# Performance work log

Hardware: AMD Instinct MI355X
Metric: run time of the kernel (lower is better)

The kernel has to match this reference:

```python
import jax, jax.numpy as jnp
import numpy as np

NUM_HEADS = 16
KV_CHANNELS = 128
MASK_FILL = -10000.0  # TE attention_mask_func fill value


def setup_inputs() -> dict:
    key = jax.random.key(0)
    k1, k2, k3 = jax.random.split(key, 3)
    S, B, H = 2048, 2, 2048
    hidden_states = jax.random.normal(k1, (S, B, H), dtype=jnp.float32)
    attention_mask = jnp.zeros((B, 1, S, S), dtype=bool)  # True = masked out
    qkv_weight = jax.random.normal(k2, (H, 3 * H), dtype=jnp.float32) * (1.0 / np.sqrt(H))
    qkv_bias = jnp.zeros((3 * H,), dtype=jnp.float32)
    proj_weight = jax.random.normal(k3, (H, H), dtype=jnp.float32) * (1.0 / np.sqrt(H))
    proj_bias = jnp.zeros((H,), dtype=jnp.float32)
    return {
        "hidden_states": hidden_states,
        "attention_mask": attention_mask,
        "qkv_weight": qkv_weight,
        "qkv_bias": qkv_bias,
        "proj_weight": proj_weight,
        "proj_bias": proj_bias,
    }


def reference(hidden_states, attention_mask, qkv_weight, qkv_bias, proj_weight, proj_bias):
    S, B, H = hidden_states.shape
    nh, d = NUM_HEADS, KV_CHANNELS
    # QKV GEMM: [s,b,H] @ [H,3H] -> [s,b,3H] -> [s,b,nh,3d] -> split
    mixed = hidden_states @ qkv_weight + qkv_bias
    mixed = mixed.reshape(S, B, nh, 3 * d)
    q, k, v = jnp.split(mixed, 3, axis=-1)  # each [s,b,nh,d]
    # BMM1 with 1/sqrt(d) scaling (layer_number=None -> no layer scaling)
    norm_factor = jnp.asarray(np.sqrt(d), dtype=hidden_states.dtype)
    scores = jnp.einsum("sbhd,tbhd->bhst", q, k) / norm_factor  # [b,nh,s,s]
    # causal mask (future positions masked) OR'd with provided bool padding mask
    causal = ~jnp.tril(jnp.ones((S, S), dtype=bool))  # True above diagonal
    mask = jnp.logical_or(causal[None, None], attention_mask)
    scores = jnp.where(mask, jnp.asarray(MASK_FILL, scores.dtype), scores)
    probs = jax.nn.softmax(scores, axis=-1)
    # dropout is identity in eval mode (training=False)
    # BMM2: [b,nh,s,t] x [t,b,nh,d] -> [s,b,nh,d] -> [s,b,H]
    context = jnp.einsum("bhst,tbhd->sbhd", probs, v).reshape(S, B, H)
    # output projection; TE Dense(use_bias=False, return_bias=True) returns bias
    out = context @ proj_weight
    return out, proj_bias
```

## Files before the change

kernel.cpp:

```cpp
#include <hip/hip_runtime.h>
#include <cstdint>
#include <math.h>

#define S_LEN 2048
#define BATCH 2
#define HID   2048
#define NHEAD 16
#define DHEAD 128

typedef _Float16 h8 __attribute__((ext_vector_type(8)));
typedef _Float16 h4 __attribute__((ext_vector_type(4)));
typedef float f32x4 __attribute__((ext_vector_type(4)));

__device__ __forceinline__ void gload16(const void* g, void* l) {
  __builtin_amdgcn_global_load_lds(
      (const __attribute__((address_space(1))) unsigned int*)g,
      (__attribute__((address_space(3))) unsigned int*)l, 16, 0, 0);
}

template <bool HAS_BIAS, bool OUT_HALF>
__global__ __launch_bounds__(256) void gemm_mfma(
    const _Float16* __restrict__ A, const _Float16* __restrict__ Bt,
    const float* __restrict__ bias, void* __restrict__ Cout, int M, int N,
    int K) {
  __shared__ _Float16 As[128 * 32];
  __shared__ _Float16 Bs[128 * 32];
  const int tid = threadIdx.x;
  const int wave = tid >> 6, lane = tid & 63;
  const int ln = lane & 15, quad = lane >> 4;
  const int wm = wave & 1, wn = wave >> 1;
  const int bm = blockIdx.y * 128, bn = blockIdx.x * 128;

  const int sr = lane >> 2;
  const int sk = (lane & 3) * 8;
  const _Float16* ga0 = A + (size_t)(bm + 32 * wave + sr) * K + sk;
  const _Float16* ga1 = A + (size_t)(bm + 32 * wave + 16 + sr) * K + sk;
  const _Float16* gb0 = Bt + (size_t)(bn + 32 * wave + sr) * K + sk;
  const _Float16* gb1 = Bt + (size_t)(bn + 32 * wave + 16 + sr) * K + sk;
  _Float16* la0 = As + 1024 * wave;
  _Float16* la1 = As + 1024 * wave + 512;
  _Float16* lb0 = Bs + 1024 * wave;
  _Float16* lb1 = Bs + 1024 * wave + 512;

  f32x4 acc[4][4];
#pragma unroll
  for (int i = 0; i < 4; i++)
#pragma unroll
    for (int j = 0; j < 4; j++) acc[i][j] = (f32x4){0.f, 0.f, 0.f, 0.f};

  for (int kt = 0; kt < K; kt += 32) {
    __syncthreads();
    gload16(ga0 + kt, la0);
    gload16(ga1 + kt, la1);
    gload16(gb0 + kt, lb0);
    gload16(gb1 + kt, lb1);
    __syncthreads();

    h8 af[4], bf[4];
#pragma unroll
    for (int mt = 0; mt < 4; mt++)
      af[mt] = *(const h8*)&As[(wm * 64 + mt * 16 + ln) * 32 + quad * 8];
#pragma unroll
    for (int nt = 0; nt < 4; nt++)
      bf[nt] = *(const h8*)&Bs[(wn * 64 + nt * 16 + ln) * 32 + quad * 8];
#pragma unroll
    for (int mt = 0; mt < 4; mt++)
#pragma unroll
      for (int nt = 0; nt < 4; nt++)
        acc[mt][nt] = __builtin_amdgcn_mfma_f32_16x16x32_f16(
            af[mt], bf[nt], acc[mt][nt], 0, 0, 0);
  }

#pragma unroll
  for (int mt = 0; mt < 4; mt++) {
#pragma unroll
    for (int r = 0; r < 4; r++) {
      const size_t row = (size_t)(bm + wm * 64 + mt * 16 + quad * 4 + r);
#pragma unroll
      for (int nt = 0; nt < 4; nt++) {
        const int col = bn + wn * 64 + nt * 16 + ln;
        float v = acc[mt][nt][r];
        if (HAS_BIAS) v += bias[col];
        if (OUT_HALF)
          ((_Float16*)Cout)[row * N + col] = (_Float16)v;
        else
          ((float*)Cout)[row * N + col] = v;
      }
    }
  }
}

__global__ __launch_bounds__(256) void transpose_cvt(
    const float* __restrict__ in, _Float16* __restrict__ out, int K, int N) {
  __shared__ float t[64][65];
  const int bn = blockIdx.x * 64, bk = blockIdx.y * 64;
  const int l = threadIdx.x & 63, g = threadIdx.x >> 6;
#pragma unroll
  for (int i = 0; i < 16; i++) {
    int r = g + 4 * i;
    t[r][l] = in[(size_t)(bk + r) * N + bn + l];
  }
  __syncthreads();
#pragma unroll
  for (int i = 0; i < 16; i++) {
    int r = g + 4 * i;
    out[(size_t)(bn + r) * K + bk + l] = (_Float16)t[l][r];
  }
}

__global__ __launch_bounds__(256) void cvt_fp16(const float* __restrict__ in,
                                                _Float16* __restrict__ out,
                                                int n4) {
  int i = blockIdx.x * blockDim.x + threadIdx.x;
  if (i < n4) {
    float4 v = ((const float4*)in)[i];
    h4 o = {(_Float16)v.x, (_Float16)v.y, (_Float16)v.z, (_Float16)v.w};
    *(h4*)&out[4 * (size_t)i] = o;
  }
}

__global__ __launch_bounds__(256) void transpose_v(
    const _Float16* __restrict__ mixed, _Float16* __restrict__ Vtg) {
  __shared__ _Float16 T[64 * 72];
  const int sb = blockIdx.x * 64;
  const int db = blockIdx.y * 64;
  const int z = blockIdx.z;
  const int tid = threadIdx.x;

  const int r = tid >> 2, d0 = (tid & 3) * 16;
  {
    const _Float16* src =
        mixed + ((size_t)(sb + r) * (BATCH * NHEAD) + z) * 384 + 256 + db + d0;
    h8 v0 = *(const h8*)src;
    h8 v1 = *(const h8*)(src + 8);
#pragma unroll
    for (int e = 0; e < 8; e++) T[(d0 + e) * 72 + r] = v0[e];
#pragma unroll
    for (int e = 0; e < 8; e++) T[(d0 + 8 + e) * 72 + r] = v1[e];
  }
  __syncthreads();
  {
    const int dl = tid >> 2, s0 = (tid & 3) * 16;
    h8 v0 = *(const h8*)&T[dl * 72 + s0];
    h8 v1 = *(const h8*)&T[dl * 72 + s0 + 8];
    _Float16* dst = Vtg + ((size_t)z * DHEAD + db + dl) * S_LEN + sb + s0;
    *(h8*)dst = v0;
    *(h8*)(dst + 8) = v1;
  }
}

__global__ __launch_bounds__(256) void flash_attn_v5(
    const _Float16* __restrict__ mixed, const _Float16* __restrict__ Vtg,
    const unsigned char* __restrict__ mask, _Float16* __restrict__ ctx) {
  const int qt = (int)gridDim.x - 1 - (int)blockIdx.x;
  const int h = blockIdx.y, b = blockIdx.z;
  const int qb = qt * 64;
  const int tid = threadIdx.x;
  const int wave = tid >> 6, lane = tid & 63;
  const int ln = lane & 15, quad = lane >> 4;

  __shared__ _Float16 Ks[32 * 136];
  __shared__ _Float16 Vt[128 * 40];
  __shared__ _Float16 St[4][16 * 40];

  const size_t RS = (size_t)BATCH * NHEAD * 384;
  const _Float16* base = mixed + ((size_t)b * NHEAD + h) * 384;
  const _Float16* vbase = Vtg + (size_t)(b * NHEAD + h) * DHEAD * S_LEN;
  const unsigned char* mbase = mask + (size_t)b * S_LEN * S_LEN;
  const float scale = 0.08838834764831845f;

  h8 qfrag[4];
  {
    const size_t row = (size_t)(qb + 16 * wave + ln);
#pragma unroll
    for (int kq = 0; kq < 4; kq++) {
      h8 v = *(const h8*)(base + row * RS + 32 * kq + 8 * quad);
#pragma unroll
      for (int j = 0; j < 8; j++) v[j] = (_Float16)((float)v[j] * scale);
      qfrag[kq] = v;
    }
  }

  f32x4 o[8];
#pragma unroll
  for (int nt = 0; nt < 8; nt++) o[nt] = (f32x4){0.f, 0.f, 0.f, 0.f};
  float lpart[4] = {0.f, 0.f, 0.f, 0.f};

  const int ntiles = 2 * qt + 2;

  const int kr = tid >> 3, kd0 = (tid & 7) * 16;
  const int vd = tid >> 1, vk0 = (tid & 1) * 16;

  for (int kt = 0; kt < ntiles; kt++) {
    const int kb = kt * 32;
    __syncthreads();

    {
      const _Float16* src = base + (size_t)(kb + kr) * RS + 128 + kd0;
      *(h8*)&Ks[kr * 136 + kd0] = *(const h8*)src;
      *(h8*)&Ks[kr * 136 + kd0 + 8] = *(const h8*)(src + 8);
    }
    {
      const _Float16* src = vbase + (size_t)vd * S_LEN + kb + vk0;
      *(h8*)&Vt[vd * 40 + vk0] = *(const h8*)src;
      *(h8*)&Vt[vd * 40 + vk0 + 8] = *(const h8*)(src + 8);
    }
    __syncthreads();

    unsigned char mreg[4][2];
#pragma unroll
    for (int r = 0; r < 4; r++)
#pragma unroll
      for (int jn = 0; jn < 2; jn++)
        mreg[r][jn] = mbase[(size_t)(qb + 16 * wave + 4 * quad + r) * S_LEN +
                            kb + 16 * jn + ln];

    f32x4 s[2];
    s[0] = (f32x4){0.f, 0.f, 0.f, 0.f};
    s[1] = (f32x4){0.f, 0.f, 0.f, 0.f};
#pragma unroll
    for (int kq = 0; kq < 4; kq++) {
#pragma unroll
      for (int jn = 0; jn < 2; jn++) {
        h8 bk = *(const h8*)&Ks[(16 * jn + ln) * 136 + 32 * kq + 8 * quad];
        s[jn] = __builtin_amdgcn_mfma_f32_16x16x32_f16(qfrag[kq], bk, s[jn], 0,
                                                       0, 0);
      }
    }

#pragma unroll
    for (int jn = 0; jn < 2; jn++)
#pragma unroll
      for (int r = 0; r < 4; r++) {
        const int grow = qb + 16 * wave + 4 * quad + r;
        const int gcol = kb + 16 * jn + ln;
        const float sv = ((gcol > grow) || mreg[r][jn]) ? -10000.0f : s[jn][r];
        const float p = __expf(sv);
        lpart[r] += p;
        St[wave][(4 * quad + r) * 40 + 16 * jn + ln] = (_Float16)p;
      }
    __threadfence_block();

    {
      h8 ap = *(const h8*)&St[wave][ln * 40 + 8 * quad];
#pragma unroll
      for (int nt = 0; nt < 8; nt++) {
        h8 bv = *(const h8*)&Vt[(16 * nt + ln) * 40 + 8 * quad];
        o[nt] =
            __builtin_amdgcn_mfma_f32_16x16x32_f16(ap, bv, o[nt], 0, 0, 0);
      }
    }
  }

#pragma unroll
  for (int r = 0; r < 4; r++) {
    float l = lpart[r];
#pragma unroll
    for (int off = 8; off >= 1; off >>= 1) l += __shfl_xor(l, off, 16);
    const float inv_l = 1.0f / l;
    const size_t row_g = (size_t)(qb + 16 * wave + 4 * quad + r);
    _Float16* dst = ctx + (row_g * BATCH + b) * HID + h * DHEAD;
#pragma unroll
    for (int nt = 0; nt < 8; nt++)
      dst[16 * nt + ln] = (_Float16)(o[nt][r] * inv_l);
  }
}

__global__ void copy_bias(const float* __restrict__ src,
                          float* __restrict__ dst) {
  int i = blockIdx.x * blockDim.x + threadIdx.x;
  if (i < HID) dst[i] = src[i];
}

extern "C" void kernel_launch(void* const* d_in, const int* in_sizes, int n_in,
                              void* d_out, int out_size, void* d_ws,
                              size_t ws_size, hipStream_t stream) {
  (void)in_sizes;
  (void)n_in;
  const float* hs = (const float*)d_in[0];
  const unsigned char* mask = (const unsigned char*)d_in[1];
  const float* qkv_w = (const float*)d_in[2];
  const float* qkv_b = (const float*)d_in[3];
  const float* proj_w = (const float*)d_in[4];
  const float* proj_b = (const float*)d_in[5];
  float* out = (float*)d_out;

  const size_t M = (size_t)S_LEN * BATCH;
  const size_t mixed_e = M * 3 * HID;
  const size_t qkvwt_e = (size_t)3 * HID * HID;
  const size_t hsh_e = M * HID;
  const size_t projwt_e = (size_t)HID * HID;
  const size_t ctx_e = M * HID;
  const size_t vtg_e = (size_t)BATCH * NHEAD * DHEAD * S_LEN;
  const size_t need =
      (mixed_e + qkvwt_e + hsh_e + projwt_e + ctx_e + vtg_e) * sizeof(_Float16);
  if (ws_size < need) return;

  _Float16* mixed = (_Float16*)d_ws;
  _Float16* qkv_wt = mixed + mixed_e;
  _Float16* hs_h = qkv_wt + qkvwt_e;
  _Float16* proj_wt = hs_h + hsh_e;
  _Float16* ctx = proj_wt + projwt_e;
  _Float16* vtg = ctx + ctx_e;

  cvt_fp16<<<(int)(hsh_e / 4 / 256), 256, 0, stream>>>(hs, hs_h,
                                                       (int)(hsh_e / 4));
  transpose_cvt<<<dim3(3 * HID / 64, HID / 64), 256, 0, stream>>>(
      qkv_w, qkv_wt, HID, 3 * HID);
  transpose_cvt<<<dim3(HID / 64, HID / 64), 256, 0, stream>>>(
      proj_w, proj_wt, HID, HID);

  gemm_mfma<true, true><<<dim3(3 * HID / 128, M / 128), 256, 0, stream>>>(
      hs_h, qkv_wt, qkv_b, mixed, (int)M, 3 * HID, HID);

  transpose_v<<<dim3(S_LEN / 64, DHEAD / 64, BATCH * NHEAD), 256, 0, stream>>>(
      mixed, vtg);

  flash_attn_v5<<<dim3(S_LEN / 64, NHEAD, BATCH), 256, 0, stream>>>(
      mixed, vtg, mask, ctx);

  gemm_mfma<false, false><<<dim3(HID / 128, M / 128), 256, 0, stream>>>(
      ctx, proj_wt, nullptr, out, (int)M, HID, HID);

  copy_bias<<<(HID + 255) / 256, 256, 0, stream>>>(proj_b, out + M * HID);
}
```

Measured before the change: 493.5 us.

## Pre-pack K and V into MFMA fragment order and load directly from global

Replaces the V transpose kernel with a pack kernel that writes both K and V tiles in the exact per-lane MFMA operand layout, so the attention kernel reads B fragments straight from global memory. This removes the per-tile LDS staging and both __syncthreads in the attention loop, and adds an occupancy hint of 4 blocks per CU through launch_bounds. Each wave now issues its own global loads for K/V (4x redundant across waves, relying on L2/L1 caching). The packed buffers reuse the hs_h and qkv_wt workspace regions, which are dead after the QKV GEMM.

```diff
diff --git a/kernel.cpp b/kernel.cpp
--- a/kernel.cpp
+++ b/kernel.cpp
@@ -119,53 +119,64 @@
   }
 }
 
-__global__ __launch_bounds__(256) void transpose_v(
-    const _Float16* __restrict__ mixed, _Float16* __restrict__ Vtg) {
-  __shared__ _Float16 T[64 * 72];
-  const int sb = blockIdx.x * 64;
-  const int db = blockIdx.y * 64;
-  const int z = blockIdx.z;
+__global__ __launch_bounds__(256) void pack_kv(
+    const _Float16* __restrict__ mixed, _Float16* __restrict__ KP,
+    _Float16* __restrict__ VP) {
+  __shared__ _Float16 Tv[128 * 40];
+  const int kt = blockIdx.x;
+  const int z = blockIdx.y;
+  const int kb = kt * 32;
   const int tid = threadIdx.x;
-
-  const int r = tid >> 2, d0 = (tid & 3) * 16;
+  const size_t RS = (size_t)BATCH * NHEAD * 384;
+  const _Float16* base = mixed + (size_t)z * 384;
+
   {
-    const _Float16* src =
-        mixed + ((size_t)(sb + r) * (BATCH * NHEAD) + z) * 384 + 256 + db + d0;
+    const int r = tid >> 3, d0 = (tid & 7) * 16;
+    const _Float16* src = base + (size_t)(kb + r) * RS + 256 + d0;
     h8 v0 = *(const h8*)src;
     h8 v1 = *(const h8*)(src + 8);
 #pragma unroll
-    for (int e = 0; e < 8; e++) T[(d0 + e) * 72 + r] = v0[e];
-#pragma unroll
-    for (int e = 0; e < 8; e++) T[(d0 + 8 + e) * 72 + r] = v1[e];
+    for (int e = 0; e < 8; e++) Tv[(d0 + e) * 40 + r] = v0[e];
+#pragma unroll
+    for (int e = 0; e < 8; e++) Tv[(d0 + 8 + e) * 40 + r] = v1[e];
   }
   __syncthreads();
-  {
-    const int dl = tid >> 2, s0 = (tid & 3) * 16;
-    h8 v0 = *(const h8*)&T[dl * 72 + s0];
-    h8 v1 = *(const h8*)&T[dl * 72 + s0 + 8];
-    _Float16* dst = Vtg + ((size_t)z * DHEAD + db + dl) * S_LEN + sb + s0;
-    *(h8*)dst = v0;
-    *(h8*)(dst + 8) = v1;
-  }
-}
-
-__global__ __launch_bounds__(256) void flash_attn_v5(
-    const _Float16* __restrict__ mixed, const _Float16* __restrict__ Vtg,
-    const unsigned char* __restrict__ mask, _Float16* __restrict__ ctx) {
+
+  const size_t tb = ((size_t)z * 64 + kt) * 8 * 512;
+#pragma unroll
+  for (int c = 0; c < 2; c++) {
+    const int idx = tid + 256 * c;
+    const int i = idx >> 6, l = idx & 63;
+    const int ln = l & 15, quad = l >> 4;
+    {
+      const int jn = i >> 2, kq = i & 3;
+      h8 v = *(const h8*)(base + (size_t)(kb + 16 * jn + ln) * RS + 128 +
+                          32 * kq + 8 * quad);
+      *(h8*)&KP[tb + (size_t)i * 512 + l * 8] = v;
+    }
+    {
+      h8 v = *(const h8*)&Tv[(16 * i + ln) * 40 + 8 * quad];
+      *(h8*)&VP[tb + (size_t)i * 512 + l * 8] = v;
+    }
+  }
+}
+
+__global__ __launch_bounds__(256, 4) void flash_attn_v6(
+    const _Float16* __restrict__ mixed, const _Float16* __restrict__ KP,
+    const _Float16* __restrict__ VP, const unsigned char* __restrict__ mask,
+    _Float16* __restrict__ ctx) {
   const int qt = (int)gridDim.x - 1 - (int)blockIdx.x;
   const int h = blockIdx.y, b = blockIdx.z;
+  const int z = b * NHEAD + h;
   const int qb = qt * 64;
   const int tid = threadIdx.x;
   const int wave = tid >> 6, lane = tid & 63;
   const int ln = lane & 15, quad = lane >> 4;
 
-  __shared__ _Float16 Ks[32 * 136];
-  __shared__ _Float16 Vt[128 * 40];
   __shared__ _Float16 St[4][16 * 40];
 
   const size_t RS = (size_t)BATCH * NHEAD * 384;
-  const _Float16* base = mixed + ((size_t)b * NHEAD + h) * 384;
-  const _Float16* vbase = Vtg + (size_t)(b * NHEAD + h) * DHEAD * S_LEN;
+  const _Float16* base = mixed + (size_t)z * 384;
   const unsigned char* mbase = mask + (size_t)b * S_LEN * S_LEN;
   const float scale = 0.08838834764831845f;
 
@@ -188,24 +199,9 @@
 
   const int ntiles = 2 * qt + 2;
 
-  const int kr = tid >> 3, kd0 = (tid & 7) * 16;
-  const int vd = tid >> 1, vk0 = (tid & 1) * 16;
-
   for (int kt = 0; kt < ntiles; kt++) {
     const int kb = kt * 32;
-    __syncthreads();
-
-    {
-      const _Float16* src = base + (size_t)(kb + kr) * RS + 128 + kd0;
-      *(h8*)&Ks[kr * 136 + kd0] = *(const h8*)src;
-      *(h8*)&Ks[kr * 136 + kd0 + 8] = *(const h8*)(src + 8);
-    }
-    {
-      const _Float16* src = vbase + (size_t)vd * S_LEN + kb + vk0;
-      *(h8*)&Vt[vd * 40 + vk0] = *(const h8*)src;
-      *(h8*)&Vt[vd * 40 + vk0 + 8] = *(const h8*)(src + 8);
-    }
-    __syncthreads();
+    const size_t tb = ((size_t)z * 64 + kt) * 8 * 512 + lane * 8;
 
     unsigned char mreg[4][2];
 #pragma unroll
@@ -222,7 +218,7 @@
     for (int kq = 0; kq < 4; kq++) {
 #pragma unroll
       for (int jn = 0; jn < 2; jn++) {
-        h8 bk = *(const h8*)&Ks[(16 * jn + ln) * 136 + 32 * kq + 8 * quad];
+        h8 bk = *(const h8*)&KP[tb + (size_t)(jn * 4 + kq) * 512];
         s[jn] = __builtin_amdgcn_mfma_f32_16x16x32_f16(qfrag[kq], bk, s[jn], 0,
                                                        0, 0);
       }
@@ -245,9 +241,8 @@
       h8 ap = *(const h8*)&St[wave][ln * 40 + 8 * quad];
 #pragma unroll
       for (int nt = 0; nt < 8; nt++) {
-        h8 bv = *(const h8*)&Vt[(16 * nt + ln) * 40 + 8 * quad];
-        o[nt] =
-            __builtin_amdgcn_mfma_f32_16x16x32_f16(ap, bv, o[nt], 0, 0, 0);
+        h8 bv = *(const h8*)&VP[tb + (size_t)nt * 512];
+        o[nt] = __builtin_amdgcn_mfma_f32_16x16x32_f16(ap, bv, o[nt], 0, 0, 0);
       }
     }
   }
@@ -291,9 +286,8 @@
   const size_t hsh_e = M * HID;
   const size_t projwt_e = (size_t)HID * HID;
   const size_t ctx_e = M * HID;
-  const size_t vtg_e = (size_t)BATCH * NHEAD * DHEAD * S_LEN;
   const size_t need =
-      (mixed_e + qkvwt_e + hsh_e + projwt_e + ctx_e + vtg_e) * sizeof(_Float16);
+      (mixed_e + qkvwt_e + hsh_e + projwt_e + ctx_e) * sizeof(_Float16);
   if (ws_size < need) return;
 
   _Float16* mixed = (_Float16*)d_ws;
@@ -301,7 +295,8 @@
   _Float16* hs_h = qkv_wt + qkvwt_e;
   _Float16* proj_wt = hs_h + hsh_e;
   _Float16* ctx = proj_wt + projwt_e;
-  _Float16* vtg = ctx + ctx_e;
+  _Float16* KP = hs_h;
+  _Float16* VP = qkv_wt;
 
   cvt_fp16<<<(int)(hsh_e / 4 / 256), 256, 0, stream>>>(hs, hs_h,
                                                        (int)(hsh_e / 4));
@@ -313,11 +308,10 @@
   gemm_mfma<true, true><<<dim3(3 * HID / 128, M / 128), 256, 0, stream>>>(
       hs_h, qkv_wt, qkv_b, mixed, (int)M, 3 * HID, HID);
 
-  transpose_v<<<dim3(S_LEN / 64, DHEAD / 64, BATCH * NHEAD), 256, 0, stream>>>(
-      mixed, vtg);
-
-  flash_attn_v5<<<dim3(S_LEN / 64, NHEAD, BATCH), 256, 0, stream>>>(
-      mixed, vtg, mask, ctx);
+  pack_kv<<<dim3(S_LEN / 32, BATCH * NHEAD), 256, 0, stream>>>(mixed, KP, VP);
+
+  flash_attn_v6<<<dim3(S_LEN / 64, NHEAD, BATCH), 256, 0, stream>>>(
+      mixed, KP, VP, mask, ctx);
 
   gemm_mfma<false, false><<<dim3(HID / 128, M / 128), 256, 0, stream>>>(
       ctx, proj_wt, nullptr, out, (int)M, HID, HID);
```

Measured after the change: 515.7 us. 4.5% more time.
